# Optimization experiments

Hardware: AMD Instinct MI355X
Metric: run time of the kernel (lower is better)

The kernel has to match this reference:

```python
import jax, jax.numpy as jnp
import numpy as np

B, S, D = 2, 2048, 1024
H = 16
KEY_DIM = 1024   # full projected dim; original scales by sqrt(key_dim), NOT head_dim
VAL_DIM = 1024
OUT_DIM = 1024


def setup_inputs() -> dict:
    key = jax.random.key(0)
    ks = jax.random.split(key, 11)
    s = 0.02
    return {
        "queries": jax.random.normal(ks[0], (B, S, D), jnp.float32),
        "keys": jax.random.normal(ks[1], (B, S, D), jnp.float32),
        "values": jax.random.normal(ks[2], (B, S, D), jnp.float32),
        "Wq": jax.random.normal(ks[3], (D, KEY_DIM), jnp.float32) * s,
        "bq": jnp.zeros((KEY_DIM,), jnp.float32),
        "Wk": jax.random.normal(ks[4], (D, KEY_DIM), jnp.float32) * s,
        "bk": jnp.zeros((KEY_DIM,), jnp.float32),
        "Wv": jax.random.normal(ks[5], (D, VAL_DIM), jnp.float32) * s,
        "bv": jnp.zeros((VAL_DIM,), jnp.float32),
        "Wo": jax.random.normal(ks[6], (KEY_DIM, OUT_DIM), jnp.float32) * s,
        "bo": jnp.zeros((OUT_DIM,), jnp.float32),
    }


def _split_heads(x):
    # [B, S, H*dh] -> [B, H, S, dh]
    b, s, _ = x.shape
    return x.reshape(b, s, H, -1).transpose(0, 2, 1, 3)


def reference(queries, keys, values, Wq, bq, Wk, bk, Wv, bv, Wo, bo):
    q = _split_heads(queries @ Wq + bq)   # [B,H,S,dk]
    k = _split_heads(keys @ Wk + bk)      # [B,H,S,dk]
    v = _split_heads(values @ Wv + bv)    # [B,H,S,dv]
    scale = jnp.sqrt(jnp.float32(KEY_DIM))  # full key_dim, as in the source
    scores = jnp.einsum('bhqd,bhkd->bhqk', q, k) / scale  # [B,H,S,S]
    # Source calls F.softmax with no dim; torch's legacy rule picks dim=1
    # (the heads axis) for a 4-D tensor. Reproduced faithfully.
    weights = jax.nn.softmax(scores, axis=1)
    o = jnp.einsum('bhqk,bhkd->bhqd', weights, v)          # [B,H,S,dv]
    o = o.transpose(0, 2, 1, 3).reshape(B, S, KEY_DIM)     # merge heads
    return o @ Wo + bo
```

## Files before the change

### kernel.cpp

```cpp
#include <hip/hip_runtime.h>


typedef unsigned short ushort;
typedef __attribute__((ext_vector_type(8))) short short8;
typedef __attribute__((ext_vector_type(4))) short short4v;
typedef __attribute__((ext_vector_type(4))) float f32x4;
typedef __attribute__((ext_vector_type(4))) float float4v;
typedef __attribute__((ext_vector_type(4))) unsigned int uint4v;
typedef __attribute__((ext_vector_type(2))) unsigned int uint2v;

#define MFMA32(a, b, c) __builtin_amdgcn_mfma_f32_16x16x32_bf16(a, b, c, 0, 0, 0)
#define MFMA16(a, b, c) __builtin_amdgcn_mfma_f32_16x16x16bf16_1k(a, b, c, 0, 0, 0)

#define VMCNT(N) asm volatile("s_waitcnt vmcnt(" #N ")" ::: "memory")
#define SCHEDBAR() __builtin_amdgcn_sched_barrier(0)

__device__ __forceinline__ ushort f2bf(float f) {
    unsigned u = __float_as_uint(f);
    u += 0x7fffu + ((u >> 16) & 1u);
    return (ushort)(u >> 16);
}
__device__ __forceinline__ ushort f2hf(float f) {
    union { _Float16 h; ushort u; } c;
    c.h = (_Float16)f;
    return c.u;
}
__device__ __forceinline__ float hf2f(ushort h) {
    union { ushort u; _Float16 h; } c;
    c.u = h;
    return (float)c.h;
}

__device__ __forceinline__ void gload16(const ushort* g, ushort* l) {
    __builtin_amdgcn_global_load_lds(
        (__attribute__((address_space(1))) void*)(unsigned long long)(g),
        (__attribute__((address_space(3))) void*)(l), 16, 0, 0);
}

__global__ __launch_bounds__(256) void convert_x_kernel(
    const float* __restrict__ q, const float* __restrict__ k,
    const float* __restrict__ v, ushort* __restrict__ out) {
    const size_t NPER = 4194304ull;
    size_t idx = ((size_t)blockIdx.x * 256 + threadIdx.x) * 8;
    const size_t stride = (size_t)gridDim.x * 256 * 8;
    for (; idx < 3 * NPER; idx += stride) {
        const float* src;
        size_t off;
        if (idx < NPER)          { src = q; off = idx; }
        else if (idx < 2 * NPER) { src = k; off = idx - NPER; }
        else                     { src = v; off = idx - 2 * NPER; }
        float4v a = *(const float4v*)(src + off);
        float4v b = *(const float4v*)(src + off + 4);
        union { ushort u[8]; uint4v v4; } pk;
        #pragma unroll
        for (int j = 0; j < 4; j++) { pk.u[j] = f2bf(a[j]); pk.u[4 + j] = f2bf(b[j]); }
        *(uint4v*)(out + idx) = pk.v4;
    }
}

__global__ __launch_bounds__(256) void transpose_w_kernel(
    const float* __restrict__ w0, const float* __restrict__ w1,
    const float* __restrict__ w2, const float* __restrict__ w3,
    ushort* __restrict__ Wt) {
    const float* W = blockIdx.z == 0 ? w0 : blockIdx.z == 1 ? w1 : blockIdx.z == 2 ? w2 : w3;
    ushort* out = Wt + (size_t)blockIdx.z * 1024 * 1024;
    __shared__ ushort st[64 * 72];
    int t = threadIdx.x;
    int kb = blockIdx.y * 64, nb = blockIdx.x * 64;
    int c4 = (t & 15) * 4;
    int r0 = t >> 4;
    #pragma unroll
    for (int p = 0; p < 4; p++) {
        int r = r0 + p * 16;
        float4v f = *(const float4v*)(W + (size_t)(kb + r) * 1024 + nb + c4);
        union { ushort u[4]; uint2v v2; } pk;
        #pragma unroll
        for (int j = 0; j < 4; j++) pk.u[j] = f2bf(f[j]);
        *(uint2v*)(st + r * 72 + c4) = pk.v2;
    }
    __syncthreads();
    int n = t >> 2;
    int kc = (t & 3) * 16;
    union { ushort u[16]; uint4v v4[2]; } tw;
    #pragma unroll
    for (int j = 0; j < 16; j++) tw.u[j] = st[(kc + j) * 72 + n];
    uint4v* dst = (uint4v*)(out + (size_t)(nb + n) * 1024 + kb + kc);
    dst[0] = tw.v4[0];
    dst[1] = tw.v4[1];
}

__device__ __forceinline__ void gemm_core(
    const ushort* __restrict__ A, const ushort* __restrict__ Bt,
    const float* __restrict__ bias, ushort* __restrict__ Cb,
    float* __restrict__ Cf, int mode, ushort* sA, ushort* sB) {
    int tid = threadIdx.x, lane = tid & 63, wave = tid >> 6;
    int li = lane & 15, g = lane >> 4;
    int mt = blockIdx.y * 128, nt = blockIdx.x * 128;
    int wm = (wave >> 1) * 64, wn = (wave & 1) * 64;
    f32x4 acc[4][4] = {};
    for (int k0 = 0; k0 < 1024; k0 += 64) {
        __syncthreads();
        #pragma unroll
        for (int i = 0; i < 4; i++) {
            int c = tid + i * 256;
            int row = c >> 3, chd = c & 7;
            int cg = chd ^ (row & 7);
            gload16(A + (size_t)(mt + row) * 1024 + k0 + cg * 8, sA + c * 8);
            gload16(Bt + (size_t)(nt + row) * 1024 + k0 + cg * 8, sB + c * 8);
        }
        __syncthreads();
        #pragma unroll
        for (int kk = 0; kk < 2; kk++) {
            short8 af[4], bfr[4];
            #pragma unroll
            for (int i = 0; i < 4; i++) {
                int ra = wm + i * 16 + li;
                int cb = kk * 64 + g * 16;
                af[i] = *(const short8*)((char*)sA + ra * 128 + (cb ^ ((ra & 7) << 4)));
                int rb = wn + i * 16 + li;
                bfr[i] = *(const short8*)((char*)sB + rb * 128 + (cb ^ ((rb & 7) << 4)));
            }
            #pragma unroll
            for (int mi = 0; mi < 4; mi++)
                #pragma unroll
                for (int ni = 0; ni < 4; ni++)
                    acc[mi][ni] = MFMA32(af[mi], bfr[ni], acc[mi][ni]);
        }
    }
    #pragma unroll
    for (int mi = 0; mi < 4; mi++) {
        #pragma unroll
        for (int ni = 0; ni < 4; ni++) {
            int n = nt + wn + ni * 16 + li;
            int m0 = mt + wm + mi * 16 + g * 4;
            float bv = bias[n];
            if (mode == 0) {
                #pragma unroll
                for (int r = 0; r < 4; r++)
                    Cb[(size_t)(m0 + r) * 1024 + n] = f2bf(acc[mi][ni][r] + bv);
            } else if (mode == 1) {
                int batch = m0 >> 11, mm = m0 & 2047;
                union { ushort u[4]; uint2v v2; } pk;
                #pragma unroll
                for (int r = 0; r < 4; r++) pk.u[r] = f2bf(acc[mi][ni][r] + bv);
                *(uint2v*)(Cb + (size_t)batch * 1024 * 2048 + (size_t)n * 2048 + mm) = pk.v2;
            } else {
                #pragma unroll
                for (int r = 0; r < 4; r++)
                    Cf[(size_t)(m0 + r) * 1024 + n] = acc[mi][ni][r] + bv;
            }
        }
    }
}

__global__ __launch_bounds__(256, 3) void proj_kernel(
    const ushort* __restrict__ Xb, const ushort* __restrict__ Wt,
    const float* __restrict__ bq, const float* __restrict__ bk,
    const float* __restrict__ bv, ushort* __restrict__ Qb,
    ushort* __restrict__ Kb, ushort* __restrict__ Vtb) {
    __shared__ ushort sA[128 * 64];
    __shared__ ushort sB[128 * 64];
    int z = blockIdx.z;
    const float* bias = z == 0 ? bq : (z == 1 ? bk : bv);
    ushort* out = z == 0 ? Qb : (z == 1 ? Kb : Vtb);
    gemm_core(Xb + (size_t)z * 4194304ull, Wt + (size_t)z * 1048576ull,
              bias, out, nullptr, z == 2 ? 1 : 0, sA, sB);
}

__global__ __launch_bounds__(256, 2) void outproj_kernel(
    const ushort* __restrict__ Ob, const ushort* __restrict__ Wt3,
    const float* __restrict__ bo, float* __restrict__ out) {
    __shared__ ushort sA[128 * 64];
    __shared__ ushort sB[128 * 64];
    gemm_core(Ob, Wt3, bo, nullptr, out, 2, sA, sB);
}

__global__ __launch_bounds__(256, 4) void zsum_kernel(
    const ushort* __restrict__ Qb, const ushort* __restrict__ Kb,
    ushort* __restrict__ Zln) {
    __shared__ ushort sQ[64 * 64];
    __shared__ ushort sK[128 * 64];
    int tid = threadIdx.x, lane = tid & 63, wid = tid >> 6;
    int li = lane & 15, g = lane >> 4;
    int bid = blockIdx.x;
    int swz = (bid & 7) * 128 + (bid >> 3);
    int qt = swz & 31, C = swz >> 5;
    int b = C >> 4, kg = C & 15;
    int q0 = qt * 64, k0 = kg * 128;
    const ushort* Qp = Qb + (size_t)(b * 2048 + q0) * 1024;
    const ushort* Kp = Kb + (size_t)(b * 2048 + k0) * 1024;
    f32x4 zacc[4][2] = {};
    for (int h = 0; h < 16; h++) {
        int co = h * 64;
        __syncthreads();
        #pragma unroll
        for (int i = 0; i < 2; i++) {
            int c = tid + i * 256;
            int r = c >> 3, m = c & 7;
            gload16(Qp + (size_t)r * 1024 + co + (m ^ (r & 7)) * 8, sQ + c * 8);
        }
        #pragma unroll
        for (int i = 0; i < 4; i++) {
            int c = tid + i * 256;
            int r = c >> 3, m = c & 7;
            gload16(Kp + (size_t)r * 1024 + co + (m ^ (r & 7)) * 8, sK + c * 8);
        }
        __syncthreads();
        short8 qf[4][2], kf[2][2];
        #pragma unroll
        for (int qs = 0; qs < 4; qs++)
            #pragma unroll
            for (int dc = 0; dc < 2; dc++) {
                int row = qs * 16 + li;
                qf[qs][dc] = *(const short8*)(
                    (char*)sQ + row * 128 + ((dc * 64 + g * 16) ^ ((row & 7) << 4)));
            }
        #pragma unroll
        for (int ks = 0; ks < 2; ks++)
            #pragma unroll
            for (int dc = 0; dc < 2; dc++) {
                int row = wid * 32 + ks * 16 + li;
                kf[ks][dc] = *(const short8*)(
                    (char*)sK + row * 128 + ((dc * 64 + g * 16) ^ ((row & 7) << 4)));
            }
        #pragma unroll
        for (int qs = 0; qs < 4; qs++)
            #pragma unroll
            for (int ks = 0; ks < 2; ks++) {
                f32x4 st = {0.f, 0.f, 0.f, 0.f};
                st = MFMA32(kf[ks][0], qf[qs][0], st);
                st = MFMA32(kf[ks][1], qf[qs][1], st);
                #pragma unroll
                for (int r = 0; r < 4; r++)
                    zacc[qs][ks][r] += __expf(st[r] * 0.03125f);
            }
    }
    #pragma unroll
    for (int qs = 0; qs < 4; qs++)
        #pragma unroll
        for (int ks = 0; ks < 2; ks++) {
            union { ushort u[4]; uint2v v; } pk;
            #pragma unroll
            for (int r = 0; r < 4; r++)
                pk.u[r] = f2hf(__logf(zacc[qs][ks][r]));
            *(uint2v*)(Zln + (size_t)(b * 2048 + q0 + qs * 16 + li) * 2048 +
                       k0 + wid * 32 + ks * 16 + g * 4) = pk.v;
        }
}

__global__ __launch_bounds__(256, 2) void pv_kernel(
    const ushort* __restrict__ Qb, const ushort* __restrict__ Kb,
    const ushort* __restrict__ Vt, const ushort* __restrict__ Zln,
    ushort* __restrict__ Ob) {
    __shared__ ushort S[4][2][5120];
    int tid = threadIdx.x, lane = tid & 63, wv = tid >> 6;
    int li = lane & 15, g = lane >> 4;
    int bid = blockIdx.x;
    int swz = (bid & 7) * 64 + (bid >> 3);
    int hp = swz & 3, p = swz >> 2;
    int b = p >> 6, qt = p & 63;
    int q0 = qt * 32;
    int head = hp * 4 + wv;
    short8 qf[2][2];
    #pragma unroll
    for (int qs = 0; qs < 2; qs++)
        #pragma unroll
        for (int dc = 0; dc < 2; dc++)
            qf[qs][dc] = *(const short8*)(
                Qb + (size_t)(b * 2048 + q0 + qs * 16 + li) * 1024 +
                head * 64 + dc * 32 + g * 8);
    f32x4 oacc[2][4] = {};
    const ushort* Ksrc[4];
    const ushort* Vsrc[4];
    const ushort* Zsrc[2];
    #pragma unroll
    for (int i = 0; i < 4; i++) {
        int c = lane + i * 64;
        int kr = c >> 3, km = c & 7;
        Ksrc[i] = Kb + (size_t)(b * 2048 + kr) * 1024 + head * 64 + (km ^ (kr & 7)) * 8;
        int vr = c >> 2, vm = c & 3;
        Vsrc[i] = Vt + (size_t)(b * 1024 + head * 64 + vr) * 2048 + (vm ^ ((vr >> 1) & 3)) * 8;
    }
    #pragma unroll
    for (int i = 0; i < 2; i++) {
        int c = lane + i * 64;
        int zr = c >> 2, zm = c & 3;
        Zsrc[i] = Zln + (size_t)(b * 2048 + q0 + zr) * 2048 + (zm ^ ((zr >> 1) & 3)) * 8;
    }
    #define PV_STAGE(BUF, KB)                                                  \
        {                                                                      \
            ushort* dst = S[wv][BUF];                                          \
            _Pragma("unroll") for (int i = 0; i < 4; i++)                      \
                gload16(Ksrc[i] + (size_t)(KB) * 1024, dst + (lane + i * 64) * 8); \
            _Pragma("unroll") for (int i = 0; i < 4; i++)                      \
                gload16(Vsrc[i] + (KB), dst + 2048 + (lane + i * 64) * 8);     \
            _Pragma("unroll") for (int i = 0; i < 2; i++)                      \
                gload16(Zsrc[i] + (KB), dst + 4096 + (lane + i * 64) * 8);     \
        }
    PV_STAGE(0, 0)
    for (int it = 0; it < 64; ++it) {
        int cur = it & 1;
        int kb = it * 32;
        if (it + 1 < 64) {
            PV_STAGE(cur ^ 1, kb + 32)
            VMCNT(10);
        } else {
            VMCNT(0);
        }
        SCHEDBAR();
        const char* Wb = (const char*)S[wv][cur];
        short8 kf[2][2];
        #pragma unroll
        for (int ks = 0; ks < 2; ks++)
            #pragma unroll
            for (int dc = 0; dc < 2; dc++) {
                int rk = ks * 16 + li;
                kf[ks][dc] = *(const short8*)(
                    Wb + rk * 128 + ((dc * 64 + g * 16) ^ ((rk & 7) << 4)));
            }
        short4v pf[2][2];
        #pragma unroll
        for (int qs = 0; qs < 2; qs++)
            #pragma unroll
            for (int ks = 0; ks < 2; ks++) {
                f32x4 st = {0.f, 0.f, 0.f, 0.f};
                st = MFMA32(kf[ks][0], qf[qs][0], st);
                st = MFMA32(kf[ks][1], qf[qs][1], st);
                int sl = ks * 4 + g;
                int rq = qs * 16 + li;
                union { ushort u[4]; uint2v v; } rz;
                rz.v = *(const uint2v*)(
                    Wb + 8192 + rq * 64 +
                    (((sl >> 1) ^ ((rq >> 1) & 3)) * 2 + (sl & 1)) * 8);
                float e0 = __expf(__builtin_fmaf(st[0], 0.03125f, -hf2f(rz.u[0])));
                float e1 = __expf(__builtin_fmaf(st[1], 0.03125f, -hf2f(rz.u[1])));
                float e2 = __expf(__builtin_fmaf(st[2], 0.03125f, -hf2f(rz.u[2])));
                float e3 = __expf(__builtin_fmaf(st[3], 0.03125f, -hf2f(rz.u[3])));
                unsigned a0 = __float_as_uint(e0) + 0x8000u;
                unsigned a1 = __float_as_uint(e1) + 0x8000u;
                unsigned a2 = __float_as_uint(e2) + 0x8000u;
                unsigned a3 = __float_as_uint(e3) + 0x8000u;
                union { unsigned u[2]; short4v s; } pk;
                pk.u[0] = __builtin_amdgcn_perm(a1, a0, 0x07060302u);
                pk.u[1] = __builtin_amdgcn_perm(a3, a2, 0x07060302u);
                pf[qs][ks] = pk.s;
            }
        #pragma unroll
        for (int ks = 0; ks < 2; ks++) {
            int sl = ks * 4 + g;
            #pragma unroll
            for (int ds = 0; ds < 4; ds++) {
                int rv = ds * 16 + li;
                short4v vf = *(const short4v*)(
                    Wb + 4096 + rv * 64 +
                    (((sl >> 1) ^ ((rv >> 1) & 3)) * 2 + (sl & 1)) * 8);
                oacc[0][ds] = MFMA16(pf[0][ks], vf, oacc[0][ds]);
                oacc[1][ds] = MFMA16(pf[1][ks], vf, oacc[1][ds]);
            }
        }
    }
    #undef PV_STAGE
    ushort* Oo = Ob + (size_t)(b * 2048 + q0) * 1024 + head * 64;
    #pragma unroll
    for (int qs = 0; qs < 2; qs++)
        #pragma unroll
        for (int ds = 0; ds < 4; ds++)
            #pragma unroll
            for (int r = 0; r < 4; r++)
                Oo[(size_t)(qs * 16 + g * 4 + r) * 1024 + ds * 16 + li] =
                    f2bf(oacc[qs][ds][r]);
}

extern "C" void kernel_launch(void* const* d_in, const int* in_sizes, int n_in,
                              void* d_out, int out_size, void* d_ws, size_t ws_size,
                              hipStream_t stream) {
    const float* queries = (const float*)d_in[0];
    const float* keys    = (const float*)d_in[1];
    const float* values  = (const float*)d_in[2];
    const float* Wq = (const float*)d_in[3];
    const float* bq = (const float*)d_in[4];
    const float* Wk = (const float*)d_in[5];
    const float* bk = (const float*)d_in[6];
    const float* Wv = (const float*)d_in[7];
    const float* bv = (const float*)d_in[8];
    const float* Wo = (const float*)d_in[9];
    const float* bo = (const float*)d_in[10];
    float* out = (float*)d_out;

    ushort* Xb  = (ushort*)d_ws;
    ushort* Wt  = Xb + 12ull * 1024 * 1024;
    ushort* Qb  = Wt + 4ull * 1024 * 1024;
    ushort* Kb  = Qb + 4ull * 1024 * 1024;
    ushort* Vtb = Kb + 4ull * 1024 * 1024;
    ushort* Zln = Xb;
    ushort* Ob  = Xb + 8ull * 1024 * 1024;

    convert_x_kernel<<<2048, 256, 0, stream>>>(queries, keys, values, Xb);
    transpose_w_kernel<<<dim3(16, 16, 4), 256, 0, stream>>>(Wq, Wk, Wv, Wo, Wt);
    proj_kernel<<<dim3(8, 32, 3), 256, 0, stream>>>(Xb, Wt, bq, bk, bv, Qb, Kb, Vtb);
    zsum_kernel<<<1024, 256, 0, stream>>>(Qb, Kb, Zln);
    pv_kernel<<<512, 256, 0, stream>>>(Qb, Kb, Vtb, Zln, Ob);
    outproj_kernel<<<dim3(8, 32), 256, 0, stream>>>(Ob, Wt + 3ull * 1024 * 1024, bo, out);
}
```

Baseline: 181.7 us.

## Load K fragments directly into registers and double-buffer them in PV loop

The PV kernel no longer stages K tiles through LDS. Each lane now loads its MFMA K operand straight from global memory into registers, using a two-way register double buffer across an unrolled-by-two loop, which shrinks the per-wave LDS buffers to hold only V and Zln. The compute body moves into a helper that raises wave priority around the MFMA groups with s_setprio. The aim is to cut LDS traffic and footprint, but the direct global K loads are less coalesced and add register pressure.

```diff
diff --git a/kernel.cpp b/kernel.cpp
--- a/kernel.cpp
+++ b/kernel.cpp
@@ -248,11 +248,68 @@
         }
 }
 
+__device__ __forceinline__ void pv_compute(
+    const short8 (&kr)[2][2], const short8 (&qf)[2][2],
+    const ushort* sbuf, int li, int g, f32x4 (&oacc)[2][4]) {
+    const char* Wb = (const char*)sbuf;
+    f32x4 st[2][2];
+    __builtin_amdgcn_s_setprio(1);
+    #pragma unroll
+    for (int qs = 0; qs < 2; qs++)
+        #pragma unroll
+        for (int ks = 0; ks < 2; ks++) {
+            f32x4 t = {0.f, 0.f, 0.f, 0.f};
+            t = MFMA32(kr[ks][0], qf[qs][0], t);
+            t = MFMA32(kr[ks][1], qf[qs][1], t);
+            st[qs][ks] = t;
+        }
+    __builtin_amdgcn_s_setprio(0);
+    short4v pf[2][2];
+    #pragma unroll
+    for (int qs = 0; qs < 2; qs++)
+        #pragma unroll
+        for (int ks = 0; ks < 2; ks++) {
+            int sl = ks * 4 + g;
+            int rq = qs * 16 + li;
+            union { ushort u[4]; uint2v v; } rz;
+            rz.v = *(const uint2v*)(
+                Wb + 4096 + rq * 64 +
+                (((sl >> 1) ^ ((rq >> 1) & 3)) * 2 + (sl & 1)) * 8);
+            float e0 = __expf(__builtin_fmaf(st[qs][ks][0], 0.03125f, -hf2f(rz.u[0])));
+            float e1 = __expf(__builtin_fmaf(st[qs][ks][1], 0.03125f, -hf2f(rz.u[1])));
+            float e2 = __expf(__builtin_fmaf(st[qs][ks][2], 0.03125f, -hf2f(rz.u[2])));
+            float e3 = __expf(__builtin_fmaf(st[qs][ks][3], 0.03125f, -hf2f(rz.u[3])));
+            unsigned a0 = __float_as_uint(e0) + 0x8000u;
+            unsigned a1 = __float_as_uint(e1) + 0x8000u;
+            unsigned a2 = __float_as_uint(e2) + 0x8000u;
+            unsigned a3 = __float_as_uint(e3) + 0x8000u;
+            union { unsigned u[2]; short4v s; } pk;
+            pk.u[0] = __builtin_amdgcn_perm(a1, a0, 0x07060302u);
+            pk.u[1] = __builtin_amdgcn_perm(a3, a2, 0x07060302u);
+            pf[qs][ks] = pk.s;
+        }
+    __builtin_amdgcn_s_setprio(1);
+    #pragma unroll
+    for (int ks = 0; ks < 2; ks++) {
+        int sl = ks * 4 + g;
+        #pragma unroll
+        for (int ds = 0; ds < 4; ds++) {
+            int rv = ds * 16 + li;
+            short4v vf = *(const short4v*)(
+                Wb + rv * 64 +
+                (((sl >> 1) ^ ((rv >> 1) & 3)) * 2 + (sl & 1)) * 8);
+            oacc[0][ds] = MFMA16(pf[0][ks], vf, oacc[0][ds]);
+            oacc[1][ds] = MFMA16(pf[1][ks], vf, oacc[1][ds]);
+        }
+    }
+    __builtin_amdgcn_s_setprio(0);
+}
+
 __global__ __launch_bounds__(256, 2) void pv_kernel(
     const ushort* __restrict__ Qb, const ushort* __restrict__ Kb,
     const ushort* __restrict__ Vt, const ushort* __restrict__ Zln,
     ushort* __restrict__ Ob) {
-    __shared__ ushort S[4][2][5120];
+    __shared__ ushort S[4][2][3072];
     int tid = threadIdx.x, lane = tid & 63, wv = tid >> 6;
     int li = lane & 15, g = lane >> 4;
     int bid = blockIdx.x;
@@ -270,14 +327,12 @@
                 Qb + (size_t)(b * 2048 + q0 + qs * 16 + li) * 1024 +
                 head * 64 + dc * 32 + g * 8);
     f32x4 oacc[2][4] = {};
-    const ushort* Ksrc[4];
+    const ushort* Kp = Kb + (size_t)(b * 2048 + li) * 1024 + head * 64 + g * 8;
     const ushort* Vsrc[4];
     const ushort* Zsrc[2];
     #pragma unroll
     for (int i = 0; i < 4; i++) {
         int c = lane + i * 64;
-        int kr = c >> 3, km = c & 7;
-        Ksrc[i] = Kb + (size_t)(b * 2048 + kr) * 1024 + head * 64 + (km ^ (kr & 7)) * 8;
         int vr = c >> 2, vm = c & 3;
         Vsrc[i] = Vt + (size_t)(b * 1024 + head * 64 + vr) * 2048 + (vm ^ ((vr >> 1) & 3)) * 8;
     }
@@ -291,75 +346,38 @@
         {                                                                      \
             ushort* dst = S[wv][BUF];                                          \
             _Pragma("unroll") for (int i = 0; i < 4; i++)                      \
-                gload16(Ksrc[i] + (size_t)(KB) * 1024, dst + (lane + i * 64) * 8); \
-            _Pragma("unroll") for (int i = 0; i < 4; i++)                      \
-                gload16(Vsrc[i] + (KB), dst + 2048 + (lane + i * 64) * 8);     \
+                gload16(Vsrc[i] + (KB), dst + (lane + i * 64) * 8);            \
             _Pragma("unroll") for (int i = 0; i < 2; i++)                      \
-                gload16(Zsrc[i] + (KB), dst + 4096 + (lane + i * 64) * 8);     \
-        }
+                gload16(Zsrc[i] + (KB), dst + 2048 + (lane + i * 64) * 8);     \
+        }
+    #define PV_LOADK(DST, KB)                                                  \
+        {                                                                      \
+            _Pragma("unroll") for (int ks2 = 0; ks2 < 2; ks2++)                \
+                _Pragma("unroll") for (int dc2 = 0; dc2 < 2; dc2++)            \
+                    DST[ks2][dc2] = *(const short8*)(                          \
+                        Kp + (size_t)((KB) + ks2 * 16) * 1024 + dc2 * 32);     \
+        }
+    short8 kA[2][2], kB[2][2];
+    PV_LOADK(kA, 0)
     PV_STAGE(0, 0)
-    for (int it = 0; it < 64; ++it) {
-        int cur = it & 1;
-        int kb = it * 32;
-        if (it + 1 < 64) {
-            PV_STAGE(cur ^ 1, kb + 32)
+    for (int it = 0; it < 64; it += 2) {
+        PV_STAGE(1, (it + 1) * 32)
+        PV_LOADK(kB, (it + 1) * 32)
+        VMCNT(10);
+        SCHEDBAR();
+        pv_compute(kA, qf, S[wv][0], li, g, oacc);
+        if (it + 2 < 64) {
+            PV_STAGE(0, (it + 2) * 32)
+            PV_LOADK(kA, (it + 2) * 32)
             VMCNT(10);
         } else {
             VMCNT(0);
         }
         SCHEDBAR();
-        const char* Wb = (const char*)S[wv][cur];
-        short8 kf[2][2];
-        #pragma unroll
-        for (int ks = 0; ks < 2; ks++)
-            #pragma unroll
-            for (int dc = 0; dc < 2; dc++) {
-                int rk = ks * 16 + li;
-                kf[ks][dc] = *(const short8*)(
-                    Wb + rk * 128 + ((dc * 64 + g * 16) ^ ((rk & 7) << 4)));
-            }
-        short4v pf[2][2];
-        #pragma unroll
-        for (int qs = 0; qs < 2; qs++)
-            #pragma unroll
-            for (int ks = 0; ks < 2; ks++) {
-                f32x4 st = {0.f, 0.f, 0.f, 0.f};
-                st = MFMA32(kf[ks][0], qf[qs][0], st);
-                st = MFMA32(kf[ks][1], qf[qs][1], st);
-                int sl = ks * 4 + g;
-                int rq = qs * 16 + li;
-                union { ushort u[4]; uint2v v; } rz;
-                rz.v = *(const uint2v*)(
-                    Wb + 8192 + rq * 64 +
-                    (((sl >> 1) ^ ((rq >> 1) & 3)) * 2 + (sl & 1)) * 8);
-                float e0 = __expf(__builtin_fmaf(st[0], 0.03125f, -hf2f(rz.u[0])));
-                float e1 = __expf(__builtin_fmaf(st[1], 0.03125f, -hf2f(rz.u[1])));
-                float e2 = __expf(__builtin_fmaf(st[2], 0.03125f, -hf2f(rz.u[2])));
-                float e3 = __expf(__builtin_fmaf(st[3], 0.03125f, -hf2f(rz.u[3])));
-                unsigned a0 = __float_as_uint(e0) + 0x8000u;
-                unsigned a1 = __float_as_uint(e1) + 0x8000u;
-                unsigned a2 = __float_as_uint(e2) + 0x8000u;
-                unsigned a3 = __float_as_uint(e3) + 0x8000u;
-                union { unsigned u[2]; short4v s; } pk;
-                pk.u[0] = __builtin_amdgcn_perm(a1, a0, 0x07060302u);
-                pk.u[1] = __builtin_amdgcn_perm(a3, a2, 0x07060302u);
-                pf[qs][ks] = pk.s;
-            }
-        #pragma unroll
-        for (int ks = 0; ks < 2; ks++) {
-            int sl = ks * 4 + g;
-            #pragma unroll
-            for (int ds = 0; ds < 4; ds++) {
-                int rv = ds * 16 + li;
-                short4v vf = *(const short4v*)(
-                    Wb + 4096 + rv * 64 +
-                    (((sl >> 1) ^ ((rv >> 1) & 3)) * 2 + (sl & 1)) * 8);
-                oacc[0][ds] = MFMA16(pf[0][ks], vf, oacc[0][ds]);
-                oacc[1][ds] = MFMA16(pf[1][ks], vf, oacc[1][ds]);
-            }
-        }
+        pv_compute(kB, qf, S[wv][1], li, g, oacc);
     }
     #undef PV_STAGE
+    #undef PV_LOADK
     ushort* Oo = Ob + (size_t)(b * 2048 + q0) * 1024 + head * 64;
     #pragma unroll
     for (int qs = 0; qs < 2; qs++)
```

Result: slower. 200.7 us (+10.5%).

## Double-buffer GEMM LDS tiles and switch softmax exp/log to base-2

Applied to the files above, without the earlier changes.

The shared GEMM core now keeps two LDS buffers and issues the global-to-LDS loads for the next K tile before computing the current one, using vmcnt waits and raw barriers in place of two __syncthreads per iteration. This is meant to hide global load latency behind the MFMA work. LDS use doubles, so proj_kernel's launch bound drops from 3 to 2 blocks per SM. Separately, the softmax-over-heads exponentials and logs move to exp2/log2 with the scale folded in (1/32 * log2 e), which removes a multiply per element.

```diff
diff --git a/kernel.cpp b/kernel.cpp
--- a/kernel.cpp
+++ b/kernel.cpp
@@ -12,8 +12,11 @@
 #define MFMA32(a, b, c) __builtin_amdgcn_mfma_f32_16x16x32_bf16(a, b, c, 0, 0, 0)
 #define MFMA16(a, b, c) __builtin_amdgcn_mfma_f32_16x16x16bf16_1k(a, b, c, 0, 0, 0)
 
+#define C2SCALE 0.045084220027780106f
+
 #define VMCNT(N) asm volatile("s_waitcnt vmcnt(" #N ")" ::: "memory")
 #define SCHEDBAR() __builtin_amdgcn_sched_barrier(0)
+#define BARRIER() __builtin_amdgcn_s_barrier()
 
 __device__ __forceinline__ ushort f2bf(float f) {
     unsigned u = __float_as_uint(f);
@@ -98,17 +101,31 @@
     int mt = blockIdx.y * 128, nt = blockIdx.x * 128;
     int wm = (wave >> 1) * 64, wn = (wave & 1) * 64;
     f32x4 acc[4][4] = {};
-    for (int k0 = 0; k0 < 1024; k0 += 64) {
-        __syncthreads();
-        #pragma unroll
-        for (int i = 0; i < 4; i++) {
-            int c = tid + i * 256;
-            int row = c >> 3, chd = c & 7;
-            int cg = chd ^ (row & 7);
-            gload16(A + (size_t)(mt + row) * 1024 + k0 + cg * 8, sA + c * 8);
-            gload16(Bt + (size_t)(nt + row) * 1024 + k0 + cg * 8, sB + c * 8);
-        }
-        __syncthreads();
+    #define G_STAGE(BUF, K0)                                                   \
+        {                                                                      \
+            _Pragma("unroll") for (int i = 0; i < 4; i++) {                    \
+                int c = tid + i * 256;                                         \
+                int row = c >> 3;                                              \
+                int cg = (c & 7) ^ (row & 7);                                  \
+                gload16(A + (size_t)(mt + row) * 1024 + (K0) + cg * 8,         \
+                        sA + (BUF) * 8192 + c * 8);                            \
+                gload16(Bt + (size_t)(nt + row) * 1024 + (K0) + cg * 8,        \
+                        sB + (BUF) * 8192 + c * 8);                            \
+            }                                                                  \
+        }
+    G_STAGE(0, 0)
+    int cur = 0;
+    for (int k0 = 0; k0 < 1024; k0 += 64, cur ^= 1) {
+        if (k0 + 64 < 1024) {
+            G_STAGE(cur ^ 1, k0 + 64)
+            VMCNT(8);
+        } else {
+            VMCNT(0);
+        }
+        SCHEDBAR();
+        BARRIER();
+        const char* bA = (const char*)(sA + cur * 8192);
+        const char* bB = (const char*)(sB + cur * 8192);
         #pragma unroll
         for (int kk = 0; kk < 2; kk++) {
             short8 af[4], bfr[4];
@@ -116,9 +133,9 @@
             for (int i = 0; i < 4; i++) {
                 int ra = wm + i * 16 + li;
                 int cb = kk * 64 + g * 16;
-                af[i] = *(const short8*)((char*)sA + ra * 128 + (cb ^ ((ra & 7) << 4)));
+                af[i] = *(const short8*)(bA + ra * 128 + (cb ^ ((ra & 7) << 4)));
                 int rb = wn + i * 16 + li;
-                bfr[i] = *(const short8*)((char*)sB + rb * 128 + (cb ^ ((rb & 7) << 4)));
+                bfr[i] = *(const short8*)(bB + rb * 128 + (cb ^ ((rb & 7) << 4)));
             }
             #pragma unroll
             for (int mi = 0; mi < 4; mi++)
@@ -126,7 +143,9 @@
                 for (int ni = 0; ni < 4; ni++)
                     acc[mi][ni] = MFMA32(af[mi], bfr[ni], acc[mi][ni]);
         }
-    }
+        BARRIER();
+    }
+    #undef G_STAGE
     #pragma unroll
     for (int mi = 0; mi < 4; mi++) {
         #pragma unroll
@@ -153,13 +172,13 @@
     }
 }
 
-__global__ __launch_bounds__(256, 3) void proj_kernel(
+__global__ __launch_bounds__(256, 2) void proj_kernel(
     const ushort* __restrict__ Xb, const ushort* __restrict__ Wt,
     const float* __restrict__ bq, const float* __restrict__ bk,
     const float* __restrict__ bv, ushort* __restrict__ Qb,
     ushort* __restrict__ Kb, ushort* __restrict__ Vtb) {
-    __shared__ ushort sA[128 * 64];
-    __shared__ ushort sB[128 * 64];
+    __shared__ ushort sA[2 * 128 * 64];
+    __shared__ ushort sB[2 * 128 * 64];
     int z = blockIdx.z;
     const float* bias = z == 0 ? bq : (z == 1 ? bk : bv);
     ushort* out = z == 0 ? Qb : (z == 1 ? Kb : Vtb);
@@ -170,8 +189,8 @@
 __global__ __launch_bounds__(256, 2) void outproj_kernel(
     const ushort* __restrict__ Ob, const ushort* __restrict__ Wt3,
     const float* __restrict__ bo, float* __restrict__ out) {
-    __shared__ ushort sA[128 * 64];
-    __shared__ ushort sB[128 * 64];
+    __shared__ ushort sA[2 * 128 * 64];
+    __shared__ ushort sB[2 * 128 * 64];
     gemm_core(Ob, Wt3, bo, nullptr, out, 2, sA, sB);
 }
 
@@ -232,7 +251,7 @@
                 st = MFMA32(kf[ks][1], qf[qs][1], st);
                 #pragma unroll
                 for (int r = 0; r < 4; r++)
-                    zacc[qs][ks][r] += __expf(st[r] * 0.03125f);
+                    zacc[qs][ks][r] += exp2f(st[r] * C2SCALE);
             }
     }
     #pragma unroll
@@ -242,7 +261,7 @@
             union { ushort u[4]; uint2v v; } pk;
             #pragma unroll
             for (int r = 0; r < 4; r++)
-                pk.u[r] = f2hf(__logf(zacc[qs][ks][r]));
+                pk.u[r] = f2hf(__log2f(zacc[qs][ks][r]));
             *(uint2v*)(Zln + (size_t)(b * 2048 + q0 + qs * 16 + li) * 2048 +
                        k0 + wid * 32 + ks * 16 + g * 4) = pk.v;
         }
@@ -332,10 +351,10 @@
                 rz.v = *(const uint2v*)(
                     Wb + 8192 + rq * 64 +
                     (((sl >> 1) ^ ((rq >> 1) & 3)) * 2 + (sl & 1)) * 8);
-                float e0 = __expf(__builtin_fmaf(st[0], 0.03125f, -hf2f(rz.u[0])));
-                float e1 = __expf(__builtin_fmaf(st[1], 0.03125f, -hf2f(rz.u[1])));
-                float e2 = __expf(__builtin_fmaf(st[2], 0.03125f, -hf2f(rz.u[2])));
-                float e3 = __expf(__builtin_fmaf(st[3], 0.03125f, -hf2f(rz.u[3])));
+                float e0 = exp2f(__builtin_fmaf(st[0], C2SCALE, -hf2f(rz.u[0])));
+                float e1 = exp2f(__builtin_fmaf(st[1], C2SCALE, -hf2f(rz.u[1])));
+                float e2 = exp2f(__builtin_fmaf(st[2], C2SCALE, -hf2f(rz.u[2])));
+                float e3 = exp2f(__builtin_fmaf(st[3], C2SCALE, -hf2f(rz.u[3])));
                 unsigned a0 = __float_as_uint(e0) + 0x8000u;
                 unsigned a1 = __float_as_uint(e1) + 0x8000u;
                 unsigned a2 = __float_as_uint(e2) + 0x8000u;
```

Result: slower. 201.3 us (+10.8%).
